# Performance work log

Hardware: AMD Instinct MI355X
Metric: run time of the kernel (lower is better)

## Reference

```python
import jax, jax.numpy as jnp
import numpy as np

HID, H, D = 128, 4, 32
NB, NP, NC = 60000, 2000, 4000
EM, EP, EI = 150000, 300000, 150000


def segment_softmax(logits, seg, n):
    # logits: [E, H], seg: [E] destination ids
    m = jax.ops.segment_max(logits, seg, num_segments=n)
    m = jnp.where(jnp.isfinite(m), m, 0.0)  # guard empty segments
    e = jnp.exp(logits - m[seg])
    s = jax.ops.segment_sum(e, seg, num_segments=n)
    return e / (s[seg] + 1e-16)


def layer_norm(x, g, b):
    mu = x.mean(-1, keepdims=True)
    v = ((x - mu) ** 2).mean(-1, keepdims=True)
    return (x - mu) / jnp.sqrt(v + 1e-5) * g + b


def setup_inputs():
    key = jax.random.key(0)
    ks = jax.random.split(key, 40)
    i = iter(range(40))
    nrm = lambda shape, s=1.0: jax.random.normal(ks[next(i)], shape, jnp.float32) * s
    w = lambda shape: nrm(shape, 0.05)
    inp = {
        'x_ball': nrm((NB, HID)),
        'x_player': nrm((NP, HID)),
        'x_context': nrm((NC, HID)),
        'em': jnp.stack([jax.random.randint(ks[next(i)], (EM,), 0, NP),
                         jax.random.randint(ks[next(i)], (EM,), 0, NB)]),
        'ep': jnp.stack([jax.random.randint(ks[next(i)], (EP,), 0, NB),
                         jax.random.randint(ks[next(i)], (EP,), 0, NB)]),
        'ei': jnp.stack([jax.random.randint(ks[next(i)], (EI,), 0, NB),
                         jax.random.randint(ks[next(i)], (EI,), 0, NC)]),
        'ea_p': nrm((EP, 1)),
        # GATv2Conv (player -matchup-> ball)
        'g_Wl': w((HID, HID)), 'g_Wr': w((HID, HID)), 'g_att': w((H, D)), 'g_b': jnp.zeros((HID,), jnp.float32),
        # TransformerConv (ball -recent_precedes-> ball), edge_dim=1
        't_Wq': w((HID, HID)), 't_bq': jnp.zeros((HID,), jnp.float32),
        't_Wk': w((HID, HID)), 't_bk': jnp.zeros((HID,), jnp.float32),
        't_Wv': w((HID, HID)), 't_bv': jnp.zeros((HID,), jnp.float32),
        't_We': w((1, HID)),
        't_Wskip': w((HID, HID)), 't_bskip': jnp.zeros((HID,), jnp.float32),
        # SAGEConv mean (ball -informs-> context)
        's_Wl': w((HID, HID)), 's_bl': jnp.zeros((HID,), jnp.float32), 's_Wr': w((HID, HID)),
        # per-type LayerNorms (only applied to types produced by the conv)
        'ln_ball_g': jnp.ones((HID,), jnp.float32), 'ln_ball_b': jnp.zeros((HID,), jnp.float32),
        'ln_ctx_g': jnp.ones((HID,), jnp.float32), 'ln_ctx_b': jnp.zeros((HID,), jnp.float32),
    }
    return inp


def reference(x_ball, x_player, x_context, em, ep, ei, ea_p,
              g_Wl, g_Wr, g_att, g_b,
              t_Wq, t_bq, t_Wk, t_bk, t_Wv, t_bv, t_We, t_Wskip, t_bskip,
              s_Wl, s_bl, s_Wr,
              ln_ball_g, ln_ball_b, ln_ctx_g, ln_ctx_b):
    # ---- GATv2Conv: player -> ball ----
    src, dst = em[0], em[1]
    xl = (x_player @ g_Wl).reshape(NP, H, D)   # src transform
    xr = (x_ball @ g_Wr).reshape(NB, H, D)     # dst transform
    e = xl[src] + xr[dst]                      # [EM, H, D]
    e = jnp.where(e > 0, e, 0.2 * e)           # leaky_relu(0.2)
    logit = jnp.einsum('ehd,hd->eh', e, g_att)
    alpha = segment_softmax(logit, dst, NB)
    gat = jax.ops.segment_sum(xl[src] * alpha[..., None], dst, num_segments=NB)
    gat = gat.reshape(NB, HID) + g_b

    # ---- TransformerConv: ball -> ball, edge_dim=1 ----
    src, dst = ep[0], ep[1]
    q = (x_ball @ t_Wq + t_bq).reshape(NB, H, D)
    k = (x_ball @ t_Wk + t_bk).reshape(NB, H, D)
    v = (x_ball @ t_Wv + t_bv).reshape(NB, H, D)
    ee = (ea_p @ t_We).reshape(EP, H, D)       # lin_edge (no bias)
    kj = k[src] + ee
    logit = jnp.einsum('ehd,ehd->eh', q[dst], kj) / jnp.sqrt(jnp.float32(D))
    alpha = segment_softmax(logit, dst, NB)
    tr = jax.ops.segment_sum((v[src] + ee) * alpha[..., None], dst, num_segments=NB)
    tr = tr.reshape(NB, HID) + x_ball @ t_Wskip + t_bskip  # root/skip connection

    # ---- SAGEConv mean: ball -> context ----
    src, dst = ei[0], ei[1]
    summ = jax.ops.segment_sum(x_ball[src], dst, num_segments=NC)
    cnt = jax.ops.segment_sum(jnp.ones((EI,), jnp.float32), dst, num_segments=NC)
    mean = summ / jnp.maximum(cnt, 1.0)[:, None]
    sage = mean @ s_Wl + s_bl + x_context @ s_Wr

    # ---- HeteroConv aggr='sum' + residual + per-type LayerNorm ----
    ball_out = layer_norm(gat + tr + x_ball, ln_ball_g, ln_ball_b)
    ctx_out = layer_norm(sage + x_context, ln_ctx_g, ln_ctx_b)
    # 'player' receives no messages -> passed through unchanged
    return (ball_out, ctx_out, x_player)
```

## Files before the change

### kernel.cpp

```cpp
#include <hip/hip_runtime.h>
#include <hip/hip_bf16.h>

#define NB 60000
#define NP 2000
#define NC 4000
#define EM_N 150000
#define EP_N 300000
#define EI_N 150000
#define POOL_N (EM_N + EP_N + EI_N)
#define SEG_TOT (NB + NB + NC)
#define SCAN_BLK 1024
#define NPART ((SEG_TOT + SCAN_BLK - 1) / SCAN_BLK)
#define BALL_TILES ((NB + 63) / 64)
#define PLYR_TILES ((NP + 63) / 64)
#define CTX_TILES ((NC + 63) / 64)
#define TPB 4
#define BW_CH ((BALL_TILES + TPB - 1) / TPB)
#define PW_CH ((PLYR_TILES + TPB - 1) / TPB)
#define CW_CH ((CTX_TILES + TPB - 1) / TPB)
#define GEMM_BLKS (6 * BW_CH + PW_CH + CW_CH)
#define FILL_BLKS ((POOL_N + 255) / 256)
#define COPY_BLKS ((NP * 128 + 255) / 256)
#define BBALL ((NB + 3) / 4)

#define QSCALE (0.17677669529663687f * 1.4426950408889634f)
#define LOG2E 1.4426950408889634f

typedef __hip_bfloat16 bf16;
typedef unsigned int u32;
typedef __attribute__((ext_vector_type(8))) short s8v;
typedef __attribute__((ext_vector_type(4))) float f4v;

__device__ __forceinline__ short f2bs(float f) {
    bf16 h = __float2bfloat16(f);
    return __builtin_bit_cast(short, h);
}
__device__ __forceinline__ float bsToF(short s) {
    return __builtin_bit_cast(float, ((unsigned)(unsigned short)s) << 16);
}
__device__ __forceinline__ float loF(u32 v) { return bsToF((short)(v & 0xffff)); }
__device__ __forceinline__ float hiF(u32 v) { return bsToF((short)(v >> 16)); }
__device__ __forceinline__ u32 packbf(float a, float b) {
    return (u32)(unsigned short)f2bs(a) | ((u32)(unsigned short)f2bs(b) << 16);
}
__device__ __forceinline__ void gl_lds16(const void* g, void* l) {
    __builtin_amdgcn_global_load_lds((const __attribute__((address_space(1))) void*)g,
                                     (__attribute__((address_space(3))) void*)l, 16, 0, 0);
}

__global__ void hist_wt_copy_kernel(const int* __restrict__ em, const int* __restrict__ ep,
                                    const int* __restrict__ ei, int* __restrict__ counts,
                                    const float* __restrict__ W0, const float* __restrict__ W1,
                                    const float* __restrict__ W2, const float* __restrict__ W3,
                                    const float* __restrict__ W4, const float* __restrict__ W5,
                                    const float* __restrict__ W6, const float* __restrict__ W7,
                                    ushort* __restrict__ Wt,
                                    const float* __restrict__ x_player, float* __restrict__ out) {
    if (blockIdx.x >= FILL_BLKS) {
        int t = (blockIdx.x - FILL_BLKS) * 256 + threadIdx.x;
        if (t < NP * 128) out[(size_t)(NB + NC) * 128 + t] = x_player[t];
        return;
    }
    int t = blockIdx.x * 256 + threadIdx.x;
    if (t < 8 * 16384) {
        int w = t >> 14, r = t & 16383, k = r >> 7, n = r & 127;
        const float* W = (w == 0) ? W0 : (w == 1) ? W1 : (w == 2) ? W2 : (w == 3) ? W3
                       : (w == 4) ? W4 : (w == 5) ? W5 : (w == 6) ? W6 : W7;
        int sc = (n >> 5) * 32 + ((n & 1) << 4) + ((n & 31) >> 1);
        Wt[w * 16384 + (k >> 3) * 1024 + sc * 8 + (k & 7)] = (unsigned short)f2bs(W[k * 128 + n]);
    }
    if (t < EM_N) atomicAdd(&counts[em[EM_N + t]], 1);
    else if (t < EM_N + EP_N) atomicAdd(&counts[NB + ep[EP_N + (t - EM_N)]], 1);
    else if (t < POOL_N) atomicAdd(&counts[2 * NB + ei[EI_N + (t - EM_N - EP_N)]], 1);
}

__global__ void scan_fused_kernel(const int* __restrict__ counts, int* __restrict__ offsets,
                                  int* __restrict__ cursors, int* __restrict__ gbase) {
    __shared__ int sd[256];
    __shared__ int sbase;
    int b = blockIdx.x, tid = threadIdx.x;
    int base = b * SCAN_BLK + tid * 4;
    int v[4]; int ts = 0;
#pragma unroll
    for (int j = 0; j < 4; j++) { int idx = base + j; v[j] = (idx < SEG_TOT) ? counts[idx] : 0; ts += v[j]; }
    sd[tid] = ts;
    for (int off = 1; off < 256; off <<= 1) {
        __syncthreads(); int t = (tid >= off) ? sd[tid - off] : 0;
        __syncthreads(); sd[tid] += t;
    }
    __syncthreads();
    if (tid == 255) sbase = atomicAdd(gbase, sd[255]);
    __syncthreads();
    int run = sd[tid] - ts + sbase;
#pragma unroll
    for (int j = 0; j < 4; j++) {
        int idx = base + j;
        if (idx < SEG_TOT) { offsets[idx] = run; cursors[idx] = run; }
        run += v[j];
    }
}

__global__ __launch_bounds__(256) void gemm6_fill_kernel(
    const float* __restrict__ Aball, const float* __restrict__ Aplyr, const float* __restrict__ Actx,
    const ushort* __restrict__ Wt,
    const float* __restrict__ bq, const float* __restrict__ bk,
    const float* __restrict__ bv_, const float* __restrict__ bskip, const float* __restrict__ bl,
    u32* __restrict__ xrP, u32* __restrict__ qP, u32* __restrict__ kP, u32* __restrict__ vP,
    u32* __restrict__ skipP, u32* __restrict__ xlP, u32* __restrict__ xwP,
    u32* __restrict__ ctxlinP,
    const int* __restrict__ em, const int* __restrict__ ep, const int* __restrict__ ei,
    const float* __restrict__ ea_p, int* __restrict__ cursors, int2* __restrict__ pool) {
    __shared__ ushort lds[16384];
    if (blockIdx.x >= GEMM_BLKS) {
        int t = (blockIdx.x - GEMM_BLKS) * 256 + threadIdx.x;
        int seg, s; float ea = 0.f;
        if (t < EM_N) { s = em[t]; seg = em[EM_N + t]; }
        else if (t < EM_N + EP_N) { int e = t - EM_N; s = ep[e]; seg = NB + ep[EP_N + e]; ea = ea_p[e]; }
        else if (t < POOL_N) { int e = t - EM_N - EP_N; s = ei[e]; seg = 2 * NB + ei[EI_N + e]; }
        else return;
        int pos = atomicAdd(&cursors[seg], 1);
        pool[pos] = make_int2(s, __float_as_int(ea));
        return;
    }
    const int tid = threadIdx.x;
    const int lane = tid & 63;
    const int wv = tid >> 6;
    const int quad = lane >> 4, l16 = lane & 15;

    int bid = blockIdx.x;
    int w, tile0, ntiles, M;
    const float* A;
    if (bid < 6 * BW_CH) {
        int widx = bid / BW_CH;
        w = (widx < 5) ? widx : 6;
        int chunk = bid - widx * BW_CH;
        tile0 = chunk * TPB; ntiles = min(TPB, BALL_TILES - tile0); M = NB; A = Aball;
    } else if (bid < 6 * BW_CH + PW_CH) {
        w = 5; int chunk = bid - 6 * BW_CH;
        tile0 = chunk * TPB; ntiles = min(TPB, PLYR_TILES - tile0); M = NP; A = Aplyr;
    } else {
        w = 7; int chunk = bid - 6 * BW_CH - PW_CH;
        tile0 = chunk * TPB; ntiles = min(TPB, CTX_TILES - tile0); M = NC; A = Actx;
    }
    u32* op; const float* bp = nullptr; const float* resid = nullptr; float scale = 1.f;
    switch (w) {
        case 0: op = xrP; break;
        case 1: op = qP; bp = bq; scale = QSCALE; break;
        case 2: op = kP; bp = bk; break;
        case 3: op = vP; bp = bv_; break;
        case 4: op = skipP; bp = bskip; resid = Aball; break;
        case 5: op = xlP; break;
        case 6: op = xwP; break;
        default: op = ctxlinP; bp = bl; resid = Actx; break;
    }

    {
        const ushort* src = Wt + w * 16384;
#pragma unroll
        for (int p = 0; p < 8; p++)
            gl_lds16(src + (size_t)(p * 256 + tid) * 8, lds + p * 2048 + wv * 512);
    }

    float2 bias2[4];
#pragma unroll
    for (int t = 0; t < 4; t++)
        bias2[t] = bp ? ((const float2*)bp)[t * 16 + l16] : make_float2(0.f, 0.f);

    float4 rawA[8], rawB[8];
    {
        int r0 = tile0 * 64 + wv * 16 + l16; if (r0 >= M) r0 = M - 1;
        const float* ap = A + (size_t)r0 * 128 + quad * 8;
#pragma unroll
        for (int kt = 0; kt < 4; kt++) {
            rawA[kt * 2] = ((const float4*)(ap + kt * 32))[0];
            rawA[kt * 2 + 1] = ((const float4*)(ap + kt * 32))[1];
        }
    }
    __syncthreads();

    for (int ti = 0; ti < ntiles; ti++) {
        int tilebase = (tile0 + ti) * 64;
        if (ti + 1 < ntiles) {
            int rn = tilebase + 64 + wv * 16 + l16; if (rn >= M) rn = M - 1;
            const float* ap = A + (size_t)rn * 128 + quad * 8;
#pragma unroll
            for (int kt = 0; kt < 4; kt++) {
                rawB[kt * 2] = ((const float4*)(ap + kt * 32))[0];
                rawB[kt * 2 + 1] = ((const float4*)(ap + kt * 32))[1];
            }
        }
        s8v a[4];
#pragma unroll
        for (int kt = 0; kt < 4; kt++) {
            float4 u = rawA[kt * 2], v = rawA[kt * 2 + 1];
            s8v f;
            f[0] = f2bs(u.x); f[1] = f2bs(u.y); f[2] = f2bs(u.z); f[3] = f2bs(u.w);
            f[4] = f2bs(v.x); f[5] = f2bs(v.y); f[6] = f2bs(v.z); f[7] = f2bs(v.w);
            a[kt] = f;
        }
        const int mbase = tilebase + wv * 16;
#pragma unroll
        for (int t = 0; t < 4; t++) {
            f4v alo = {0.f, 0.f, 0.f, 0.f}, ahi = {0.f, 0.f, 0.f, 0.f};
#pragma unroll
            for (int kt = 0; kt < 4; kt++) {
                s8v blo = *(const s8v*)(lds + (kt * 4 + quad) * 1024 + (t * 32 + l16) * 8);
                s8v bhi = *(const s8v*)(lds + (kt * 4 + quad) * 1024 + (t * 32 + 16 + l16) * 8);
                alo = __builtin_amdgcn_mfma_f32_16x16x32_bf16(a[kt], blo, alo, 0, 0, 0);
                ahi = __builtin_amdgcn_mfma_f32_16x16x32_bf16(a[kt], bhi, ahi, 0, 0, 0);
            }
#pragma unroll
            for (int r = 0; r < 4; r++) {
                int row = mbase + quad * 4 + r;
                if (row < M) {
                    float vlo = (alo[r] + bias2[t].x) * scale;
                    float vhi = (ahi[r] + bias2[t].y) * scale;
                    if (resid) {
                        float2 x2 = ((const float2*)resid)[(size_t)row * 64 + t * 16 + l16];
                        vlo += x2.x; vhi += x2.y;
                    }
                    op[(size_t)row * 64 + t * 16 + l16] = packbf(vlo, vhi);
                }
            }
        }
#pragma unroll
        for (int i = 0; i < 8; i++) rawA[i] = rawB[i];
    }
}

__device__ __forceinline__ void gat_batch(const u32 xv[4], const bool ok[4],
                                          float xr0, float xr1, float attx, float atty,
                                          float& n0, float& n1, float& deg) {
    float p[4], xa[4], xb[4];
#pragma unroll
    for (int i = 0; i < 4; i++) {
        xa[i] = loF(xv[i]); xb[i] = hiF(xv[i]);
        float u0 = xa[i] + xr0; u0 = u0 > 0.f ? u0 : 0.2f * u0;
        float u1 = xb[i] + xr1; u1 = u1 > 0.f ? u1 : 0.2f * u1;
        p[i] = u0 * attx + u1 * atty;
    }
#pragma unroll
    for (int m = 1; m <= 8; m <<= 1) {
#pragma unroll
        for (int i = 0; i < 4; i++) p[i] += __shfl_xor(p[i], m);
    }
#pragma unroll
    for (int i = 0; i < 4; i++) {
        p[i] = ok[i] ? exp2f(p[i]) : 0.f;
        n0 += p[i] * xa[i]; n1 += p[i] * xb[i]; deg += p[i];
    }
}

__device__ __forceinline__ void tr_batch(const u32 kk[4], const u32 vv[4],
                                         const float ea[4], const bool ok[4],
                                         float q0, float q1, float dw,
                                         float& sv0, float& sv1, float& spe, float& det) {
    float p[4];
#pragma unroll
    for (int i = 0; i < 4; i++) p[i] = q0 * loF(kk[i]) + q1 * hiF(kk[i]);
#pragma unroll
    for (int m = 1; m <= 8; m <<= 1) {
#pragma unroll
        for (int i = 0; i < 4; i++) p[i] += __shfl_xor(p[i], m);
    }
#pragma unroll
    for (int i = 0; i < 4; i++) {
        p[i] = ok[i] ? exp2f(p[i] + ea[i] * dw) : 0.f;
        sv0 += p[i] * loF(vv[i]); sv1 += p[i] * hiF(vv[i]);
        spe += p[i] * ea[i]; det += p[i];
    }
}

__global__ __launch_bounds__(256) void ball_sage_kernel(
    const u32* __restrict__ xlP, const u32* __restrict__ xrP, const u32* __restrict__ qP,
    const u32* __restrict__ kP, const u32* __restrict__ vP,
    const u32* __restrict__ skipP, const u32* __restrict__ xwP,
    const u32* __restrict__ ctxlinP,
    const float* __restrict__ g_att, const float* __restrict__ g_b, const float* __restrict__ We,
    const int* __restrict__ offsets, const int* __restrict__ counts,
    const int2* __restrict__ pool,
    const float* __restrict__ ln_g, const float* __restrict__ ln_b,
    const float* __restrict__ cg, const float* __restrict__ cb,
    float* __restrict__ out) {
    __shared__ float part[4][128];
    const int wv = threadIdx.x >> 6, l = threadIdx.x & 63;

    if (blockIdx.x >= BBALL) {
        int c = blockIdx.x - BBALL;
        int beg = offsets[2 * NB + c], cnt = counts[2 * NB + c];
        float s0 = 0.f, s1 = 0.f;
        int j = wv;
        if (j < cnt) {
            int i0 = pool[beg + j].x;
            int idx1 = (j + 4 < cnt) ? beg + j + 4 : 0;
            int i1 = pool[idx1].x;
            u32 x0 = xwP[(size_t)i0 * 64 + l];
            u32 x1 = xwP[(size_t)i1 * 64 + l];
            for (; j < cnt; j += 4) {
                int idx2 = (j + 8 < cnt) ? beg + j + 8 : 0;
                int i2 = pool[idx2].x;
                s0 += loF(x0); s1 += hiF(x0);
                x0 = x1;
                x1 = xwP[(size_t)i2 * 64 + l];
            }
        }
        part[wv][l * 2] = s0; part[wv][l * 2 + 1] = s1;
        __syncthreads();
        if (wv == 0) {
            float m = fmaxf((float)cnt, 1.f);
            u32 cl = ctxlinP[(size_t)c * 64 + l];
            float v0 = (part[0][l * 2] + part[1][l * 2] + part[2][l * 2] + part[3][l * 2]) / m + loF(cl);
            float v1 = (part[0][l * 2 + 1] + part[1][l * 2 + 1] + part[2][l * 2 + 1] + part[3][l * 2 + 1]) / m + hiF(cl);
            float s = v0 + v1;
#pragma unroll
            for (int m2 = 1; m2 <= 32; m2 <<= 1) s += __shfl_xor(s, m2);
            float mu = s * (1.f / 128.f);
            float d0 = v0 - mu, d1 = v1 - mu;
            float qv = d0 * d0 + d1 * d1;
#pragma unroll
            for (int m2 = 1; m2 <= 32; m2 <<= 1) qv += __shfl_xor(qv, m2);
            float inv = rsqrtf(qv * (1.f / 128.f) + 1e-5f);
            float2 g2 = ((const float2*)cg)[l];
            float2 b2 = ((const float2*)cb)[l];
            ((float2*)out)[(size_t)(NB + c) * 64 + l] =
                make_float2(d0 * inv * g2.x + b2.x, d1 * inv * g2.y + b2.y);
        }
        return;
    }

    const int d = blockIdx.x * 4 + wv;
    const size_t rowD = (size_t)d * 64;
    const int ds = __builtin_amdgcn_readfirstlane(d);

    u32 xr2 = xrP[rowD + l];
    u32 q2 = qP[rowD + l];
    u32 sk = skipP[rowD + l];

    const int begG = offsets[ds], cntG = counts[ds];
    const int begT = offsets[NB + ds], cntT = counts[NB + ds];
    int gS[8];
#pragma unroll
    for (int i = 0; i < 8; i++) { int idx = (i < cntG) ? begG + i : 0; gS[i] = pool[idx].x; }
    int tS[8]; float tE[8];
#pragma unroll
    for (int i = 0; i < 8; i++) {
        int idx = (i < cntT) ? begT + i : 0;
        int2 pr = pool[idx]; tS[i] = pr.x; tE[i] = __int_as_float(pr.y);
    }

    u32 gx[8];
    if (cntG > 0) {
#pragma unroll
        for (int i = 0; i < 4; i++) gx[i] = xlP[(size_t)gS[i] * 64 + l];
        if (cntG > 4) {
#pragma unroll
            for (int i = 4; i < 8; i++) gx[i] = xlP[(size_t)gS[i] * 64 + l];
        }
    }
    u32 kk[8], vv[8];
    if (cntT > 0) {
#pragma unroll
        for (int i = 0; i < 4; i++) { kk[i] = kP[(size_t)tS[i] * 64 + l]; vv[i] = vP[(size_t)tS[i] * 64 + l]; }
        if (cntT > 4) {
#pragma unroll
            for (int i = 4; i < 8; i++) { kk[i] = kP[(size_t)tS[i] * 64 + l]; vv[i] = vP[(size_t)tS[i] * 64 + l]; }
        }
    }

    float q0 = loF(q2), q1 = hiF(q2);
    float2 we = ((const float2*)We)[l];
    float dw = q0 * we.x + q1 * we.y;
#pragma unroll
    for (int m = 1; m <= 8; m <<= 1) dw += __shfl_xor(dw, m);

    float2 attv = ((const float2*)g_att)[l];
    float attx = attv.x * LOG2E, atty = attv.y * LOG2E;
    float xr0 = loF(xr2), xr1 = hiF(xr2);
    float n0 = 0.f, n1 = 0.f, deg = 0.f;
    if (cntG > 0) {
        bool ok[4];
#pragma unroll
        for (int i = 0; i < 4; i++) ok[i] = (i < cntG);
        gat_batch(&gx[0], ok, xr0, xr1, attx, atty, n0, n1, deg);
        if (cntG > 4) {
            bool ok2[4];
#pragma unroll
            for (int i = 0; i < 4; i++) ok2[i] = (4 + i < cntG);
            gat_batch(&gx[4], ok2, xr0, xr1, attx, atty, n0, n1, deg);
        }
        for (int j = 8; j < cntG; j += 4) {
            bool ok3[4]; u32 xv[4];
#pragma unroll
            for (int i = 0; i < 4; i++) {
                ok3[i] = (j + i < cntG);
                int idx = ok3[i] ? begG + j + i : 0;
                xv[i] = xlP[(size_t)pool[idx].x * 64 + l];
            }
            gat_batch(xv, ok3, xr0, xr1, attx, atty, n0, n1, deg);
        }
    }
    float gat0 = n0 / (deg + 1e-16f), gat1 = n1 / (deg + 1e-16f);

    float sv0 = 0.f, sv1 = 0.f, spe = 0.f, det = 0.f;
    if (cntT > 0) {
        bool ok[4];
#pragma unroll
        for (int i = 0; i < 4; i++) ok[i] = (i < cntT);
        tr_batch(&kk[0], &vv[0], &tE[0], ok, q0, q1, dw, sv0, sv1, spe, det);
        if (cntT > 4) {
            bool ok2[4];
#pragma unroll
            for (int i = 0; i < 4; i++) ok2[i] = (4 + i < cntT);
            tr_batch(&kk[4], &vv[4], &tE[4], ok2, q0, q1, dw, sv0, sv1, spe, det);
        }
        for (int j = 8; j < cntT; j += 4) {
            bool ok3[4]; u32 kt2[4], vt2[4]; float ea[4];
#pragma unroll
            for (int i = 0; i < 4; i++) {
                ok3[i] = (j + i < cntT);
                int idx = ok3[i] ? begT + j + i : 0;
                int2 pr = pool[idx];
                ea[i] = __int_as_float(pr.y);
                kt2[i] = kP[(size_t)pr.x * 64 + l];
                vt2[i] = vP[(size_t)pr.x * 64 + l];
            }
            tr_batch(kt2, vt2, ea, ok3, q0, q1, dw, sv0, sv1, spe, det);
        }
    }
    float tr0 = (sv0 + spe * we.x) / (det + 1e-16f);
    float tr1 = (sv1 + spe * we.y) / (det + 1e-16f);

    float2 gb2 = ((const float2*)g_b)[l];
    float val0 = loF(sk) + gb2.x + gat0 + tr0;
    float val1 = hiF(sk) + gb2.y + gat1 + tr1;
    float s = val0 + val1;
#pragma unroll
    for (int m = 1; m <= 32; m <<= 1) s += __shfl_xor(s, m);
    float mu = s * (1.f / 128.f);
    float d0 = val0 - mu, d1 = val1 - mu;
    float qv = d0 * d0 + d1 * d1;
#pragma unroll
    for (int m = 1; m <= 32; m <<= 1) qv += __shfl_xor(qv, m);
    float inv = rsqrtf(qv * (1.f / 128.f) + 1e-5f);
    float2 g2 = ((const float2*)ln_g)[l];
    float2 b2 = ((const float2*)ln_b)[l];
    ((float2*)out)[rowD + l] = make_float2(d0 * inv * g2.x + b2.x, d1 * inv * g2.y + b2.y);
}

extern "C" void kernel_launch(void* const* d_in, const int* in_sizes, int n_in,
                              void* d_out, int out_size, void* d_ws, size_t ws_size,
                              hipStream_t stream) {
    const float* x_ball = (const float*)d_in[0];
    const float* x_player = (const float*)d_in[1];
    const float* x_context = (const float*)d_in[2];
    const int* em = (const int*)d_in[3];
    const int* ep = (const int*)d_in[4];
    const int* ei = (const int*)d_in[5];
    const float* ea_p = (const float*)d_in[6];
    const float* g_Wl = (const float*)d_in[7];
    const float* g_Wr = (const float*)d_in[8];
    const float* g_att = (const float*)d_in[9];
    const float* g_b = (const float*)d_in[10];
    const float* t_Wq = (const float*)d_in[11];
    const float* t_bq = (const float*)d_in[12];
    const float* t_Wk = (const float*)d_in[13];
    const float* t_bk = (const float*)d_in[14];
    const float* t_Wv = (const float*)d_in[15];
    const float* t_bv = (const float*)d_in[16];
    const float* t_We = (const float*)d_in[17];
    const float* t_Wskip = (const float*)d_in[18];
    const float* t_bskip = (const float*)d_in[19];
    const float* s_Wl = (const float*)d_in[20];
    const float* s_bl = (const float*)d_in[21];
    const float* s_Wr = (const float*)d_in[22];
    const float* ln_ball_g = (const float*)d_in[23];
    const float* ln_ball_b = (const float*)d_in[24];
    const float* ln_ctx_g = (const float*)d_in[25];
    const float* ln_ctx_b = (const float*)d_in[26];
    float* out = (float*)d_out;

    float* ws = (float*)d_ws;
    size_t o = 0;
    int* counts = (int*)(ws + o);   o += SEG_TOT;
    int* gbase = (int*)(ws + o);    o += 1;
    int* offsets = (int*)(ws + o);  o += SEG_TOT;
    int* cursors = (int*)(ws + o);  o += SEG_TOT;
    if (o & 1) o++;
    int2* pool = (int2*)(ws + o);   o += (size_t)POOL_N * 2;
    o = (o + 3) & ~(size_t)3;
    ushort* Wt = (ushort*)(ws + o); o += (8 * 16384) / 2;
    u32* xlP = (u32*)(ws + o);      o += (size_t)NP * 64;
    u32* xrP = (u32*)(ws + o);      o += (size_t)NB * 64;
    u32* qP = (u32*)(ws + o);       o += (size_t)NB * 64;
    u32* skipP = (u32*)(ws + o);    o += (size_t)NB * 64;
    u32* xwP = (u32*)(ws + o);      o += (size_t)NB * 64;
    u32* ctxlinP = (u32*)(ws + o);  o += (size_t)NC * 64;
    u32* kP = (u32*)(ws + o);       o += (size_t)NB * 64;
    u32* vP = (u32*)(ws + o);       o += (size_t)NB * 64;

    dim3 blk(256);
    hipMemsetAsync(counts, 0, (SEG_TOT + 1) * sizeof(int), stream);
    hist_wt_copy_kernel<<<FILL_BLKS + COPY_BLKS, blk, 0, stream>>>(
        em, ep, ei, counts, g_Wr, t_Wq, t_Wk, t_Wv, t_Wskip, g_Wl, s_Wl, s_Wr, Wt, x_player, out);
    scan_fused_kernel<<<NPART, blk, 0, stream>>>(counts, offsets, cursors, gbase);
    gemm6_fill_kernel<<<GEMM_BLKS + FILL_BLKS, blk, 0, stream>>>(
        x_ball, x_player, x_context, Wt, t_bq, t_bk, t_bv, t_bskip, s_bl,
        xrP, qP, kP, vP, skipP, xlP, xwP, ctxlinP, em, ep, ei, ea_p, cursors, pool);
    ball_sage_kernel<<<BBALL + NC, blk, 0, stream>>>(
        xlP, xrP, qP, kP, vP, skipP, xwP, ctxlinP, g_att, g_b, t_We,
        offsets, counts, pool, ln_ball_g, ln_ball_b, ln_ctx_g, ln_ctx_b, out);
}
```

Before: 310.1 us.

## Pre-convert inputs to bf16, interleave K/V, replace fill atomics with ranks

The histogram kernel now records each edge's rank from its counting atomic and converts x_ball, x_context and x_player to bf16 once. The pool fill then computes positions from offsets plus rank, which removes the second round of atomics and the cursor array. The GEMMs read bf16 activations instead of re-reading and converting fp32 rows in every one of the six weight passes. K and V are stored interleaved so the transformer gather needs one 8-byte load per edge instead of two separate loads. The cost is an extra conversion pass, a write and read of the ranks array, and more workspace.

```diff
diff --git a/kernel.cpp b/kernel.cpp
--- a/kernel.cpp
+++ b/kernel.cpp
@@ -20,7 +20,10 @@
 #define CW_CH ((CTX_TILES + TPB - 1) / TPB)
 #define GEMM_BLKS (6 * BW_CH + PW_CH + CW_CH)
 #define FILL_BLKS ((POOL_N + 255) / 256)
-#define COPY_BLKS ((NP * 128 + 255) / 256)
+#define CONVB ((NB * 16 + 255) / 256)
+#define CONVC ((NC * 16 + 255) / 256)
+#define CONVP ((NP * 16 + 255) / 256)
+#define HIST_BLKS (FILL_BLKS + CONVB + CONVC + CONVP)
 #define BBALL ((NB + 3) / 4)
 
 #define QSCALE (0.17677669529663687f * 1.4426950408889634f)
@@ -50,15 +53,39 @@
 
 __global__ void hist_wt_copy_kernel(const int* __restrict__ em, const int* __restrict__ ep,
                                     const int* __restrict__ ei, int* __restrict__ counts,
+                                    int* __restrict__ ranks,
                                     const float* __restrict__ W0, const float* __restrict__ W1,
                                     const float* __restrict__ W2, const float* __restrict__ W3,
                                     const float* __restrict__ W4, const float* __restrict__ W5,
                                     const float* __restrict__ W6, const float* __restrict__ W7,
                                     ushort* __restrict__ Wt,
-                                    const float* __restrict__ x_player, float* __restrict__ out) {
+                                    const float* __restrict__ x_ball, const float* __restrict__ x_context,
+                                    const float* __restrict__ x_player,
+                                    u32* __restrict__ xbB, u32* __restrict__ xbC, u32* __restrict__ xbP,
+                                    float* __restrict__ out) {
     if (blockIdx.x >= FILL_BLKS) {
-        int t = (blockIdx.x - FILL_BLKS) * 256 + threadIdx.x;
-        if (t < NP * 128) out[(size_t)(NB + NC) * 128 + t] = x_player[t];
+        int b2 = blockIdx.x - FILL_BLKS;
+        if (b2 < CONVB) {
+            int idx = b2 * 256 + threadIdx.x;
+            const float4* p = (const float4*)(x_ball + (size_t)idx * 8);
+            float4 u = p[0], v = p[1];
+            ((uint4*)xbB)[idx] = make_uint4(packbf(u.x, u.y), packbf(u.z, u.w),
+                                            packbf(v.x, v.y), packbf(v.z, v.w));
+        } else if (b2 < CONVB + CONVC) {
+            int idx = (b2 - CONVB) * 256 + threadIdx.x;
+            const float4* p = (const float4*)(x_context + (size_t)idx * 8);
+            float4 u = p[0], v = p[1];
+            ((uint4*)xbC)[idx] = make_uint4(packbf(u.x, u.y), packbf(u.z, u.w),
+                                            packbf(v.x, v.y), packbf(v.z, v.w));
+        } else {
+            int idx = (b2 - CONVB - CONVC) * 256 + threadIdx.x;
+            const float4* p = (const float4*)(x_player + (size_t)idx * 8);
+            float4 u = p[0], v = p[1];
+            ((uint4*)xbP)[idx] = make_uint4(packbf(u.x, u.y), packbf(u.z, u.w),
+                                            packbf(v.x, v.y), packbf(v.z, v.w));
+            float4* po = (float4*)(out + (size_t)(NB + NC) * 128 + (size_t)idx * 8);
+            po[0] = u; po[1] = v;
+        }
         return;
     }
     int t = blockIdx.x * 256 + threadIdx.x;
@@ -69,13 +96,13 @@
         int sc = (n >> 5) * 32 + ((n & 1) << 4) + ((n & 31) >> 1);
         Wt[w * 16384 + (k >> 3) * 1024 + sc * 8 + (k & 7)] = (unsigned short)f2bs(W[k * 128 + n]);
     }
-    if (t < EM_N) atomicAdd(&counts[em[EM_N + t]], 1);
-    else if (t < EM_N + EP_N) atomicAdd(&counts[NB + ep[EP_N + (t - EM_N)]], 1);
-    else if (t < POOL_N) atomicAdd(&counts[2 * NB + ei[EI_N + (t - EM_N - EP_N)]], 1);
+    if (t < EM_N) ranks[t] = atomicAdd(&counts[em[EM_N + t]], 1);
+    else if (t < EM_N + EP_N) ranks[t] = atomicAdd(&counts[NB + ep[EP_N + (t - EM_N)]], 1);
+    else if (t < POOL_N) ranks[t] = atomicAdd(&counts[2 * NB + ei[EI_N + (t - EM_N - EP_N)]], 1);
 }
 
 __global__ void scan_fused_kernel(const int* __restrict__ counts, int* __restrict__ offsets,
-                                  int* __restrict__ cursors, int* __restrict__ gbase) {
+                                  int* __restrict__ gbase) {
     __shared__ int sd[256];
     __shared__ int sbase;
     int b = blockIdx.x, tid = threadIdx.x;
@@ -95,21 +122,23 @@
 #pragma unroll
     for (int j = 0; j < 4; j++) {
         int idx = base + j;
-        if (idx < SEG_TOT) { offsets[idx] = run; cursors[idx] = run; }
+        if (idx < SEG_TOT) offsets[idx] = run;
         run += v[j];
     }
 }
 
 __global__ __launch_bounds__(256) void gemm6_fill_kernel(
-    const float* __restrict__ Aball, const float* __restrict__ Aplyr, const float* __restrict__ Actx,
+    const u32* __restrict__ xbB, const u32* __restrict__ xbP, const u32* __restrict__ xbC,
+    const float* __restrict__ Aball, const float* __restrict__ Actx,
     const ushort* __restrict__ Wt,
     const float* __restrict__ bq, const float* __restrict__ bk,
     const float* __restrict__ bv_, const float* __restrict__ bskip, const float* __restrict__ bl,
-    u32* __restrict__ xrP, u32* __restrict__ qP, u32* __restrict__ kP, u32* __restrict__ vP,
+    u32* __restrict__ xrP, u32* __restrict__ qP, u32* __restrict__ kvP,
     u32* __restrict__ skipP, u32* __restrict__ xlP, u32* __restrict__ xwP,
     u32* __restrict__ ctxlinP,
     const int* __restrict__ em, const int* __restrict__ ep, const int* __restrict__ ei,
-    const float* __restrict__ ea_p, int* __restrict__ cursors, int2* __restrict__ pool) {
+    const float* __restrict__ ea_p, const int* __restrict__ offsets,
+    const int* __restrict__ ranks, int2* __restrict__ pool) {
     __shared__ ushort lds[16384];
     if (blockIdx.x >= GEMM_BLKS) {
         int t = (blockIdx.x - GEMM_BLKS) * 256 + threadIdx.x;
@@ -118,7 +147,7 @@
         else if (t < EM_N + EP_N) { int e = t - EM_N; s = ep[e]; seg = NB + ep[EP_N + e]; ea = ea_p[e]; }
         else if (t < POOL_N) { int e = t - EM_N - EP_N; s = ei[e]; seg = 2 * NB + ei[EI_N + e]; }
         else return;
-        int pos = atomicAdd(&cursors[seg], 1);
+        int pos = offsets[seg] + ranks[t];
         pool[pos] = make_int2(s, __float_as_int(ea));
         return;
     }
@@ -129,25 +158,26 @@
 
     int bid = blockIdx.x;
     int w, tile0, ntiles, M;
-    const float* A;
+    const u32* A;
     if (bid < 6 * BW_CH) {
         int widx = bid / BW_CH;
         w = (widx < 5) ? widx : 6;
         int chunk = bid - widx * BW_CH;
-        tile0 = chunk * TPB; ntiles = min(TPB, BALL_TILES - tile0); M = NB; A = Aball;
+        tile0 = chunk * TPB; ntiles = min(TPB, BALL_TILES - tile0); M = NB; A = xbB;
     } else if (bid < 6 * BW_CH + PW_CH) {
         w = 5; int chunk = bid - 6 * BW_CH;
-        tile0 = chunk * TPB; ntiles = min(TPB, PLYR_TILES - tile0); M = NP; A = Aplyr;
+        tile0 = chunk * TPB; ntiles = min(TPB, PLYR_TILES - tile0); M = NP; A = xbP;
     } else {
         w = 7; int chunk = bid - 6 * BW_CH - PW_CH;
-        tile0 = chunk * TPB; ntiles = min(TPB, CTX_TILES - tile0); M = NC; A = Actx;
+        tile0 = chunk * TPB; ntiles = min(TPB, CTX_TILES - tile0); M = NC; A = xbC;
     }
     u32* op; const float* bp = nullptr; const float* resid = nullptr; float scale = 1.f;
+    int ostride = 64, omul = 1, ooff = 0;
     switch (w) {
         case 0: op = xrP; break;
         case 1: op = qP; bp = bq; scale = QSCALE; break;
-        case 2: op = kP; bp = bk; break;
-        case 3: op = vP; bp = bv_; break;
+        case 2: op = kvP; bp = bk; ostride = 128; omul = 2; ooff = 0; break;
+        case 3: op = kvP; bp = bv_; ostride = 128; omul = 2; ooff = 1; break;
         case 4: op = skipP; bp = bskip; resid = Aball; break;
         case 5: op = xlP; break;
         case 6: op = xwP; break;
@@ -166,15 +196,12 @@
     for (int t = 0; t < 4; t++)
         bias2[t] = bp ? ((const float2*)bp)[t * 16 + l16] : make_float2(0.f, 0.f);
 
-    float4 rawA[8], rawB[8];
+    s8v aCur[4], aNext[4];
     {
         int r0 = tile0 * 64 + wv * 16 + l16; if (r0 >= M) r0 = M - 1;
-        const float* ap = A + (size_t)r0 * 128 + quad * 8;
-#pragma unroll
-        for (int kt = 0; kt < 4; kt++) {
-            rawA[kt * 2] = ((const float4*)(ap + kt * 32))[0];
-            rawA[kt * 2 + 1] = ((const float4*)(ap + kt * 32))[1];
-        }
+        const s8v* ap = (const s8v*)(A + (size_t)r0 * 64 + quad * 4);
+#pragma unroll
+        for (int kt = 0; kt < 4; kt++) aCur[kt] = ap[kt * 4];
     }
     __syncthreads();
 
@@ -182,21 +209,9 @@
         int tilebase = (tile0 + ti) * 64;
         if (ti + 1 < ntiles) {
             int rn = tilebase + 64 + wv * 16 + l16; if (rn >= M) rn = M - 1;
-            const float* ap = A + (size_t)rn * 128 + quad * 8;
-#pragma unroll
-            for (int kt = 0; kt < 4; kt++) {
-                rawB[kt * 2] = ((const float4*)(ap + kt * 32))[0];
-                rawB[kt * 2 + 1] = ((const float4*)(ap + kt * 32))[1];
-            }
-        }
-        s8v a[4];
-#pragma unroll
-        for (int kt = 0; kt < 4; kt++) {
-            float4 u = rawA[kt * 2], v = rawA[kt * 2 + 1];
-            s8v f;
-            f[0] = f2bs(u.x); f[1] = f2bs(u.y); f[2] = f2bs(u.z); f[3] = f2bs(u.w);
-            f[4] = f2bs(v.x); f[5] = f2bs(v.y); f[6] = f2bs(v.z); f[7] = f2bs(v.w);
-            a[kt] = f;
+            const s8v* ap = (const s8v*)(A + (size_t)rn * 64 + quad * 4);
+#pragma unroll
+            for (int kt = 0; kt < 4; kt++) aNext[kt] = ap[kt * 4];
         }
         const int mbase = tilebase + wv * 16;
 #pragma unroll
@@ -206,8 +221,8 @@
             for (int kt = 0; kt < 4; kt++) {
                 s8v blo = *(const s8v*)(lds + (kt * 4 + quad) * 1024 + (t * 32 + l16) * 8);
                 s8v bhi = *(const s8v*)(lds + (kt * 4 + quad) * 1024 + (t * 32 + 16 + l16) * 8);
-                alo = __builtin_amdgcn_mfma_f32_16x16x32_bf16(a[kt], blo, alo, 0, 0, 0);
-                ahi = __builtin_amdgcn_mfma_f32_16x16x32_bf16(a[kt], bhi, ahi, 0, 0, 0);
+                alo = __builtin_amdgcn_mfma_f32_16x16x32_bf16(aCur[kt], blo, alo, 0, 0, 0);
+                ahi = __builtin_amdgcn_mfma_f32_16x16x32_bf16(aCur[kt], bhi, ahi, 0, 0, 0);
             }
 #pragma unroll
             for (int r = 0; r < 4; r++) {
@@ -219,12 +234,12 @@
                         float2 x2 = ((const float2*)resid)[(size_t)row * 64 + t * 16 + l16];
                         vlo += x2.x; vhi += x2.y;
                     }
-                    op[(size_t)row * 64 + t * 16 + l16] = packbf(vlo, vhi);
+                    op[(size_t)row * ostride + (size_t)(t * 16 + l16) * omul + ooff] = packbf(vlo, vhi);
                 }
             }
         }
 #pragma unroll
-        for (int i = 0; i < 8; i++) rawA[i] = rawB[i];
+        for (int i = 0; i < 4; i++) aCur[i] = aNext[i];
     }
 }
 
@@ -251,13 +266,12 @@
     }
 }
 
-__device__ __forceinline__ void tr_batch(const u32 kk[4], const u32 vv[4],
-                                         const float ea[4], const bool ok[4],
+__device__ __forceinline__ void tr_batch(const uint2 kv[4], const float ea[4], const bool ok[4],
                                          float q0, float q1, float dw,
                                          float& sv0, float& sv1, float& spe, float& det) {
     float p[4];
 #pragma unroll
-    for (int i = 0; i < 4; i++) p[i] = q0 * loF(kk[i]) + q1 * hiF(kk[i]);
+    for (int i = 0; i < 4; i++) p[i] = q0 * loF(kv[i].x) + q1 * hiF(kv[i].x);
 #pragma unroll
     for (int m = 1; m <= 8; m <<= 1) {
 #pragma unroll
@@ -266,15 +280,14 @@
 #pragma unroll
     for (int i = 0; i < 4; i++) {
         p[i] = ok[i] ? exp2f(p[i] + ea[i] * dw) : 0.f;
-        sv0 += p[i] * loF(vv[i]); sv1 += p[i] * hiF(vv[i]);
+        sv0 += p[i] * loF(kv[i].y); sv1 += p[i] * hiF(kv[i].y);
         spe += p[i] * ea[i]; det += p[i];
     }
 }
 
 __global__ __launch_bounds__(256) void ball_sage_kernel(
     const u32* __restrict__ xlP, const u32* __restrict__ xrP, const u32* __restrict__ qP,
-    const u32* __restrict__ kP, const u32* __restrict__ vP,
-    const u32* __restrict__ skipP, const u32* __restrict__ xwP,
+    const uint2* __restrict__ kvP, const u32* __restrict__ skipP, const u32* __restrict__ xwP,
     const u32* __restrict__ ctxlinP,
     const float* __restrict__ g_att, const float* __restrict__ g_b, const float* __restrict__ We,
     const int* __restrict__ offsets, const int* __restrict__ counts,
@@ -357,13 +370,13 @@
             for (int i = 4; i < 8; i++) gx[i] = xlP[(size_t)gS[i] * 64 + l];
         }
     }
-    u32 kk[8], vv[8];
+    uint2 kva[8];
     if (cntT > 0) {
 #pragma unroll
-        for (int i = 0; i < 4; i++) { kk[i] = kP[(size_t)tS[i] * 64 + l]; vv[i] = vP[(size_t)tS[i] * 64 + l]; }
+        for (int i = 0; i < 4; i++) kva[i] = kvP[(size_t)tS[i] * 64 + l];
         if (cntT > 4) {
 #pragma unroll
-            for (int i = 4; i < 8; i++) { kk[i] = kP[(size_t)tS[i] * 64 + l]; vv[i] = vP[(size_t)tS[i] * 64 + l]; }
+            for (int i = 4; i < 8; i++) kva[i] = kvP[(size_t)tS[i] * 64 + l];
         }
     }
 
@@ -406,25 +419,24 @@
         bool ok[4];
 #pragma unroll
         for (int i = 0; i < 4; i++) ok[i] = (i < cntT);
-        tr_batch(&kk[0], &vv[0], &tE[0], ok, q0, q1, dw, sv0, sv1, spe, det);
+        tr_batch(&kva[0], &tE[0], ok, q0, q1, dw, sv0, sv1, spe, det);
         if (cntT > 4) {
             bool ok2[4];
 #pragma unroll
             for (int i = 0; i < 4; i++) ok2[i] = (4 + i < cntT);
-            tr_batch(&kk[4], &vv[4], &tE[4], ok2, q0, q1, dw, sv0, sv1, spe, det);
+            tr_batch(&kva[4], &tE[4], ok2, q0, q1, dw, sv0, sv1, spe, det);
         }
         for (int j = 8; j < cntT; j += 4) {
-            bool ok3[4]; u32 kt2[4], vt2[4]; float ea[4];
+            bool ok3[4]; uint2 kv[4]; float ea[4];
 #pragma unroll
             for (int i = 0; i < 4; i++) {
                 ok3[i] = (j + i < cntT);
                 int idx = ok3[i] ? begT + j + i : 0;
                 int2 pr = pool[idx];
                 ea[i] = __int_as_float(pr.y);
-                kt2[i] = kP[(size_t)pr.x * 64 + l];
-                vt2[i] = vP[(size_t)pr.x * 64 + l];
+                kv[i] = kvP[(size_t)pr.x * 64 + l];
             }
-            tr_batch(kt2, vt2, ea, ok3, q0, q1, dw, sv0, sv1, spe, det);
+            tr_batch(kv, ea, ok3, q0, q1, dw, sv0, sv1, spe, det);
         }
     }
     float tr0 = (sv0 + spe * we.x) / (det + 1e-16f);
@@ -484,29 +496,33 @@
     int* counts = (int*)(ws + o);   o += SEG_TOT;
     int* gbase = (int*)(ws + o);    o += 1;
     int* offsets = (int*)(ws + o);  o += SEG_TOT;
-    int* cursors = (int*)(ws + o);  o += SEG_TOT;
+    int* ranks = (int*)(ws + o);    o += POOL_N;
     if (o & 1) o++;
     int2* pool = (int2*)(ws + o);   o += (size_t)POOL_N * 2;
     o = (o + 3) & ~(size_t)3;
     ushort* Wt = (ushort*)(ws + o); o += (8 * 16384) / 2;
+    u32* xbB = (u32*)(ws + o);      o += (size_t)NB * 64;
+    u32* xbC = (u32*)(ws + o);      o += (size_t)NC * 64;
+    u32* xbP = (u32*)(ws + o);      o += (size_t)NP * 64;
     u32* xlP = (u32*)(ws + o);      o += (size_t)NP * 64;
     u32* xrP = (u32*)(ws + o);      o += (size_t)NB * 64;
     u32* qP = (u32*)(ws + o);       o += (size_t)NB * 64;
     u32* skipP = (u32*)(ws + o);    o += (size_t)NB * 64;
     u32* xwP = (u32*)(ws + o);      o += (size_t)NB * 64;
     u32* ctxlinP = (u32*)(ws + o);  o += (size_t)NC * 64;
-    u32* kP = (u32*)(ws + o);       o += (size_t)NB * 64;
-    u32* vP = (u32*)(ws + o);       o += (size_t)NB * 64;
+    if (o & 1) o++;
+    u32* kvP = (u32*)(ws + o);      o += (size_t)NB * 128;
 
     dim3 blk(256);
     hipMemsetAsync(counts, 0, (SEG_TOT + 1) * sizeof(int), stream);
-    hist_wt_copy_kernel<<<FILL_BLKS + COPY_BLKS, blk, 0, stream>>>(
-        em, ep, ei, counts, g_Wr, t_Wq, t_Wk, t_Wv, t_Wskip, g_Wl, s_Wl, s_Wr, Wt, x_player, out);
-    scan_fused_kernel<<<NPART, blk, 0, stream>>>(counts, offsets, cursors, gbase);
+    hist_wt_copy_kernel<<<HIST_BLKS, blk, 0, stream>>>(
+        em, ep, ei, counts, ranks, g_Wr, t_Wq, t_Wk, t_Wv, t_Wskip, g_Wl, s_Wl, s_Wr, Wt,
+        x_ball, x_context, x_player, xbB, xbC, xbP, out);
+    scan_fused_kernel<<<NPART, blk, 0, stream>>>(counts, offsets, gbase);
     gemm6_fill_kernel<<<GEMM_BLKS + FILL_BLKS, blk, 0, stream>>>(
-        x_ball, x_player, x_context, Wt, t_bq, t_bk, t_bv, t_bskip, s_bl,
-        xrP, qP, kP, vP, skipP, xlP, xwP, ctxlinP, em, ep, ei, ea_p, cursors, pool);
+        xbB, xbP, xbC, x_ball, x_context, Wt, t_bq, t_bk, t_bv, t_bskip, s_bl,
+        xrP, qP, kvP, skipP, xlP, xwP, ctxlinP, em, ep, ei, ea_p, offsets, ranks, pool);
     ball_sage_kernel<<<BBALL + NC, blk, 0, stream>>>(
-        xlP, xrP, qP, kP, vP, skipP, xwP, ctxlinP, g_att, g_b, t_We,
+        xlP, xrP, qP, (const uint2*)kvP, skipP, xwP, ctxlinP, g_att, g_b, t_We,
         offsets, counts, pool, ln_ball_g, ln_ball_b, ln_ctx_g, ln_ctx_b, out);
 }
```

Measured after the change: 303.7 us. 1.02x faster.
